# Optimization experiments

Measured on AMD Instinct MI355X. Metric: run time of the kernel, lower is better.

Reference implementation:

```python
import jax, jax.numpy as jnp
import numpy as np

DIM = 512
HEADS = 8
HEAD_DIM = DIM // HEADS
HIDDEN = 4 * DIM
EPS = 1e-5


def _ln(x, g, b):
    mu = jnp.mean(x, axis=-1, keepdims=True)
    var = jnp.mean((x - mu) ** 2, axis=-1, keepdims=True)
    return (x - mu) * jax.lax.rsqrt(var + EPS) * g + b


def setup_inputs() -> dict:
    key = jax.random.key(0)
    ks = jax.random.split(key, 12)
    s = lambda fan: 1.0 / np.sqrt(fan)
    return {
        "x": jax.random.normal(ks[0], (2, 4096, DIM), jnp.float32),
        "ln1_g": jnp.ones((DIM,), jnp.float32),
        "ln1_b": jnp.zeros((DIM,), jnp.float32),
        "ln2_g": jnp.ones((DIM,), jnp.float32),
        "ln2_b": jnp.zeros((DIM,), jnp.float32),
        "qkv_w": jax.random.normal(ks[1], (3 * DIM, DIM), jnp.float32) * s(DIM),
        "qkv_b": jnp.zeros((3 * DIM,), jnp.float32),
        "proj_w": jax.random.normal(ks[2], (DIM, DIM), jnp.float32) * s(DIM),
        "proj_b": jnp.zeros((DIM,), jnp.float32),
        "fc1_w": jax.random.normal(ks[3], (HIDDEN, DIM), jnp.float32) * s(DIM),
        "fc1_b": jnp.zeros((HIDDEN,), jnp.float32),
        "fc2_w": jax.random.normal(ks[4], (DIM, HIDDEN), jnp.float32) * s(HIDDEN),
        "fc2_b": jnp.zeros((DIM,), jnp.float32),
    }


def reference(x, ln1_g, ln1_b, ln2_g, ln2_b, qkv_w, qkv_b, proj_w, proj_b,
              fc1_w, fc1_b, fc2_w, fc2_b):
    B, N, C = x.shape
    # --- attention (pre-norm) ---
    h = _ln(x, ln1_g, ln1_b)
    qkv = h @ qkv_w.T + qkv_b                      # [B,N,3C]
    qkv = qkv.reshape(B, N, 3, HEADS, HEAD_DIM)
    q, k, v = (jnp.moveaxis(qkv, 2, 0)[i].transpose(0, 2, 1, 3) for i in range(3))  # [B,H,N,D]
    scale = HEAD_DIM ** -0.5
    attn = jax.nn.softmax(jnp.einsum('bhnd,bhmd->bhnm', q, k) * scale, axis=-1)
    out = jnp.einsum('bhnm,bhmd->bhnd', attn, v)   # [B,H,N,D]
    out = out.transpose(0, 2, 1, 3).reshape(B, N, C)
    x = x + out @ proj_w.T + proj_b
    # --- MLP (pre-norm) ---
    h = _ln(x, ln2_g, ln2_b)
    h = jax.nn.gelu(h @ fc1_w.T + fc1_b, approximate=False)
    return x + h @ fc2_w.T + fc2_b
```

## Files before the change

kernel.cpp:

```cpp
#include <hip/hip_runtime.h>
#include <hip/hip_bf16.h>
#include <string.h>

using bf16 = __hip_bfloat16;
typedef __attribute__((ext_vector_type(8))) short short8;
typedef __attribute__((ext_vector_type(4))) float f32x4;

#define GAS __attribute__((address_space(1)))
#define LAS __attribute__((address_space(3)))

__device__ __forceinline__ void gld_lds16(const void* g, void* l) {
  __builtin_amdgcn_global_load_lds((const GAS void*)g, (LAS void*)l, 16, 0, 0);
}

__device__ __forceinline__ unsigned short f2bfu(float f) {
  bf16 h = __float2bfloat16(f);
  return *reinterpret_cast<unsigned short*>(&h);
}

__device__ __forceinline__ unsigned pack_bf16x2(float lo, float hi) {
  __hip_bfloat162 v = __float22bfloat162_rn(make_float2(lo, hi));
  unsigned u;
  __builtin_memcpy(&u, &v, 4);
  return u;
}

__global__ __launch_bounds__(256) void cvt_all(const float* __restrict__ w0, bf16* __restrict__ o0,
                                               const float* __restrict__ w1, bf16* __restrict__ o1,
                                               const float* __restrict__ w2, bf16* __restrict__ o2,
                                               const float* __restrict__ w3, bf16* __restrict__ o3) {
  int i = blockIdx.x * 256 + threadIdx.x;
  const float* src; bf16* dst; int off;
  if (i < 196608)      { src = w0; dst = o0; off = i; }
  else if (i < 262144) { src = w1; dst = o1; off = i - 196608; }
  else if (i < 524288) { src = w2; dst = o2; off = i - 262144; }
  else                 { src = w3; dst = o3; off = i - 524288; }
  float4 v = reinterpret_cast<const float4*>(src)[off];
  ushort4 o;
  o.x = f2bfu(v.x); o.y = f2bfu(v.y); o.z = f2bfu(v.z); o.w = f2bfu(v.w);
  reinterpret_cast<ushort4*>(dst)[off] = o;
}

__global__ __launch_bounds__(256) void ln_kernel(const float* __restrict__ x,
                                                 const float* __restrict__ g,
                                                 const float* __restrict__ b,
                                                 bf16* __restrict__ out) {
  const int row = blockIdx.x * 4 + (threadIdx.x >> 6);
  const int lane = threadIdx.x & 63;
  const float4* xr = reinterpret_cast<const float4*>(x + (size_t)row * 512);
  float4 v0 = xr[lane], v1 = xr[64 + lane];
  float s  = v0.x + v0.y + v0.z + v0.w + v1.x + v1.y + v1.z + v1.w;
  float s2 = v0.x*v0.x + v0.y*v0.y + v0.z*v0.z + v0.w*v0.w
           + v1.x*v1.x + v1.y*v1.y + v1.z*v1.z + v1.w*v1.w;
  #pragma unroll
  for (int d = 1; d < 64; d <<= 1) { s += __shfl_xor(s, d); s2 += __shfl_xor(s2, d); }
  const float mu = s * (1.0f / 512.0f);
  const float var = s2 * (1.0f / 512.0f) - mu * mu;
  const float rstd = rsqrtf(var + 1e-5f);
  const float4* g4 = reinterpret_cast<const float4*>(g);
  const float4* b4 = reinterpret_cast<const float4*>(b);
  float4 ga = g4[lane], gb = g4[64 + lane], ba = b4[lane], bb = b4[64 + lane];
  ushort4 o0, o1;
  o0.x = f2bfu((v0.x - mu) * rstd * ga.x + ba.x);
  o0.y = f2bfu((v0.y - mu) * rstd * ga.y + ba.y);
  o0.z = f2bfu((v0.z - mu) * rstd * ga.z + ba.z);
  o0.w = f2bfu((v0.w - mu) * rstd * ga.w + ba.w);
  o1.x = f2bfu((v1.x - mu) * rstd * gb.x + bb.x);
  o1.y = f2bfu((v1.y - mu) * rstd * gb.y + bb.y);
  o1.z = f2bfu((v1.z - mu) * rstd * gb.z + bb.z);
  o1.w = f2bfu((v1.w - mu) * rstd * gb.w + bb.w);
  ushort4* orow = reinterpret_cast<ushort4*>(out + (size_t)row * 512);
  orow[lane] = o0;
  orow[64 + lane] = o1;
}

template <int EPI>
__global__ __launch_bounds__(256) void gemm_bt(const bf16* __restrict__ A,
                                               const bf16* __restrict__ B,
                                               const float* __restrict__ bias,
                                               const float* __restrict__ resid,
                                               void* __restrict__ Cv,
                                               int M, int N, int K) {
  __shared__ bf16 As[128 * 32];
  __shared__ bf16 Bs[128 * 32];
  const int tid = threadIdx.x;
  const int lane = tid & 63, wid = tid >> 6;
  const int lr = lane & 15, lg = lane >> 4;
  const int row0 = blockIdx.x * 128, col0 = blockIdx.y * 128;
  const int wr = (wid >> 1) * 64, wc = (wid & 1) * 64;
  f32x4 acc[4][4] = {};
  const int r1 = tid >> 2,          c1 = (tid & 3) * 8;
  const int r2 = (256 + tid) >> 2,  c2 = ((256 + tid) & 3) * 8;
  for (int kt = 0; kt < K; kt += 32) {
    __syncthreads();
    gld_lds16(A + (size_t)(row0 + r1) * K + kt + c1, As + tid * 8);
    gld_lds16(A + (size_t)(row0 + r2) * K + kt + c2, As + (256 + tid) * 8);
    gld_lds16(B + (size_t)(col0 + r1) * K + kt + c1, Bs + tid * 8);
    gld_lds16(B + (size_t)(col0 + r2) * K + kt + c2, Bs + (256 + tid) * 8);
    __syncthreads();
    short8 af[4], bfr[4];
    #pragma unroll
    for (int mi = 0; mi < 4; ++mi)
      af[mi] = *reinterpret_cast<const short8*>(&As[(wr + mi * 16 + lr) * 32 + lg * 8]);
    #pragma unroll
    for (int nj = 0; nj < 4; ++nj)
      bfr[nj] = *reinterpret_cast<const short8*>(&Bs[(wc + nj * 16 + lr) * 32 + lg * 8]);
    #pragma unroll
    for (int mi = 0; mi < 4; ++mi)
      #pragma unroll
      for (int nj = 0; nj < 4; ++nj)
        acc[mi][nj] = __builtin_amdgcn_mfma_f32_16x16x32_bf16(af[mi], bfr[nj], acc[mi][nj], 0, 0, 0);
  }
  #pragma unroll
  for (int mi = 0; mi < 4; ++mi) {
    #pragma unroll
    for (int nj = 0; nj < 4; ++nj) {
      const int col = col0 + wc + nj * 16 + lr;
      const float bv = bias ? bias[col] : 0.0f;
      #pragma unroll
      for (int rg = 0; rg < 4; ++rg) {
        const int row = row0 + wr + mi * 16 + lg * 4 + rg;
        float v = acc[mi][nj][rg] + bv;
        if constexpr (EPI == 1) v = 0.5f * v * (1.0f + erff(v * 0.70710678118654752f));
        if constexpr (EPI == 2) {
          reinterpret_cast<float*>(Cv)[(size_t)row * N + col] = v + resid[(size_t)row * N + col];
        } else {
          reinterpret_cast<bf16*>(Cv)[(size_t)row * N + col] = __float2bfloat16(v);
        }
      }
    }
  }
}

template <int EPI>
__global__ __launch_bounds__(256) void gemm_bt64(const bf16* __restrict__ A,
                                                 const bf16* __restrict__ B,
                                                 const float* __restrict__ bias,
                                                 const float* __restrict__ resid,
                                                 void* __restrict__ Cv,
                                                 int M, int N, int K) {
  __shared__ bf16 As[64 * 64];
  __shared__ bf16 Bs[64 * 64];
  const int tid = threadIdx.x;
  const int lane = tid & 63, wid = tid >> 6;
  const int lr = lane & 15, lg = lane >> 4;
  const int row0 = blockIdx.x * 64, col0 = blockIdx.y * 64;
  const int wr = (wid >> 1) * 32, wc = (wid & 1) * 32;
  f32x4 acc[2][2] = {};
  const int xsw = (lr & 7) << 4;
  const int fb0 = lr * 128 + ((lg * 16) ^ xsw);
  const int fb1 = lr * 128 + ((64 + lg * 16) ^ xsw);
  const int ph0 = tid * 16, ph1 = (256 + tid) * 16;
  const int r0 = ph0 >> 7, r1 = ph1 >> 7;
  const int lb0 = ph0 ^ ((r0 & 7) << 4), lb1 = ph1 ^ ((r1 & 7) << 4);
  const char* Ab0 = (const char*)A + (size_t)(row0 + r0) * K * 2 + (lb0 & 127);
  const char* Ab1 = (const char*)A + (size_t)(row0 + r1) * K * 2 + (lb1 & 127);
  const char* Bb0 = (const char*)B + (size_t)(col0 + r0) * K * 2 + (lb0 & 127);
  const char* Bb1 = (const char*)B + (size_t)(col0 + r1) * K * 2 + (lb1 & 127);
  for (int kt = 0; kt < K; kt += 64) {
    __syncthreads();
    gld_lds16(Ab0 + kt * 2, (char*)As + ph0);
    gld_lds16(Ab1 + kt * 2, (char*)As + ph1);
    gld_lds16(Bb0 + kt * 2, (char*)Bs + ph0);
    gld_lds16(Bb1 + kt * 2, (char*)Bs + ph1);
    __syncthreads();
    short8 af0[2], af1[2], bf0[2], bf1[2];
    #pragma unroll
    for (int mi = 0; mi < 2; ++mi) {
      af0[mi] = *reinterpret_cast<const short8*>((const char*)As + (wr + mi * 16) * 128 + fb0);
      af1[mi] = *reinterpret_cast<const short8*>((const char*)As + (wr + mi * 16) * 128 + fb1);
    }
    #pragma unroll
    for (int nj = 0; nj < 2; ++nj) {
      bf0[nj] = *reinterpret_cast<const short8*>((const char*)Bs + (wc + nj * 16) * 128 + fb0);
      bf1[nj] = *reinterpret_cast<const short8*>((const char*)Bs + (wc + nj * 16) * 128 + fb1);
    }
    #pragma unroll
    for (int mi = 0; mi < 2; ++mi)
      #pragma unroll
      for (int nj = 0; nj < 2; ++nj) {
        acc[mi][nj] = __builtin_amdgcn_mfma_f32_16x16x32_bf16(af0[mi], bf0[nj], acc[mi][nj], 0, 0, 0);
        acc[mi][nj] = __builtin_amdgcn_mfma_f32_16x16x32_bf16(af1[mi], bf1[nj], acc[mi][nj], 0, 0, 0);
      }
  }
  #pragma unroll
  for (int mi = 0; mi < 2; ++mi) {
    #pragma unroll
    for (int nj = 0; nj < 2; ++nj) {
      const int col = col0 + wc + nj * 16 + lr;
      const float bv = bias ? bias[col] : 0.0f;
      #pragma unroll
      for (int rg = 0; rg < 4; ++rg) {
        const int row = row0 + wr + mi * 16 + lg * 4 + rg;
        float v = acc[mi][nj][rg] + bv;
        if constexpr (EPI == 1) v = 0.5f * v * (1.0f + erff(v * 0.70710678118654752f));
        if constexpr (EPI == 2) {
          reinterpret_cast<float*>(Cv)[(size_t)row * N + col] = v + resid[(size_t)row * N + col];
        } else {
          reinterpret_cast<bf16*>(Cv)[(size_t)row * N + col] = __float2bfloat16(v);
        }
      }
    }
  }
}

__global__ __launch_bounds__(256) void reshape_qkv(const bf16* __restrict__ C,
                                                   bf16* __restrict__ q,
                                                   bf16* __restrict__ k,
                                                   bf16* __restrict__ vf) {
  const int nt = blockIdx.x;
  const int bh = blockIdx.y;
  const int b = bh >> 3, h = bh & 7;
  __shared__ bf16 vs[64][65];
  const int tid = threadIdx.x;
  const float qs = 0.125f * 1.44269504088896340736f;
  #pragma unroll
  for (int i = 0; i < 16; ++i) {
    const int idx = i * 256 + tid;
    const int rr = idx >> 6, c = idx & 63;
    const size_t crow = ((size_t)b * 4096 + nt * 64 + rr) * 1536;
    const size_t onb = ((size_t)bh * 4096 + nt * 64 + rr) * 64 + c;
    q[onb] = __float2bfloat16(__bfloat162float(C[crow + h * 64 + c]) * qs);
    k[onb] = C[crow + 512 + h * 64 + c];
    vs[c][rr] = C[crow + 1024 + h * 64 + c];
  }
  __syncthreads();
  #pragma unroll
  for (int i = 0; i < 2; ++i) {
    const int slot = i * 256 + tid;
    const int db = slot >> 7, kk = (slot >> 6) & 1, l = slot & 63;
    const int lr = l & 15, lg = l >> 4;
    const short8 wv = *reinterpret_cast<const short8*>(&vs[db * 16 + lr][kk * 32 + lg * 8]);
    bf16* dst = vf + ((size_t)bh * 64 + nt) * 4096 + (size_t)(db * 2 + kk) * 512 + l * 8;
    *reinterpret_cast<short8*>(dst) = wv;
  }
}

__global__ __launch_bounds__(256, 4) void attn_kernel(const bf16* __restrict__ Q,
                                                      const bf16* __restrict__ K,
                                                      const bf16* __restrict__ Vf,
                                                      bf16* __restrict__ Out) {
  const int qt = blockIdx.x;
  const int bh = blockIdx.y;
  const int b = bh >> 3, h = bh & 7;
  __shared__ bf16 QP[4096];
  __shared__ bf16 Ks[2][4096];
  const int tid = threadIdx.x, wid = tid >> 6, lane = tid & 63;
  const int lr = lane & 15, lg = lane >> 4;
  const int xsw = (lr & 7) << 4;
  const int fb0 = lr * 128 + ((lg * 16) ^ xsw);
  const int fb1 = lr * 128 + ((64 + lg * 16) ^ xsw);
  const char* Qg = (const char*)(Q + ((size_t)bh * 4096 + qt * 64) * 64);
  const char* Kg = (const char*)(K + (size_t)bh * 4096 * 64);
  const char* vlb = (const char*)Vf + (size_t)bh * 524288 + lane * 16;
  const int ph0 = tid * 16, ph1 = (256 + tid) * 16;
  const int sr0 = ph0 >> 7, sr1 = ph1 >> 7;
  const int lb0 = ph0 ^ ((sr0 & 7) << 4), lb1 = ph1 ^ ((sr1 & 7) << 4);
  int vK0 = lb0, vK1 = lb1;

  gld_lds16(Qg + lb0, (char*)QP + ph0);
  gld_lds16(Qg + lb1, (char*)QP + ph1);
  gld_lds16(Kg + vK0, (char*)Ks[0] + ph0);
  gld_lds16(Kg + vK1, (char*)Ks[0] + ph1);
  vK0 += 8192; vK1 += 8192;
  __syncthreads();
  const char* bpA0 = (const char*)QP + wid * 2048 + fb0;
  const char* bpA1 = (const char*)QP + wid * 2048 + fb1;
  const short8 bq0 = *reinterpret_cast<const short8*>(bpA0);
  const short8 bq1 = *reinterpret_cast<const short8*>(bpA1);
  char* pwp[4];
  #pragma unroll
  for (int nk = 0; nk < 4; ++nk)
    pwp[nk] = (char*)QP + wid * 2048 + lr * 128 + ((nk * 32 + lg * 8) ^ xsw);

  f32x4 Oa[4] = {};
  float mrow = -1e30f, lrow = 0.0f;
  int toff = 0;

#define ATTN_STAGE(BUF) do {                                   \
    gld_lds16(Kg + vK0, (char*)Ks[BUF] + ph0);                 \
    gld_lds16(Kg + vK1, (char*)Ks[BUF] + ph1);                 \
    vK0 += 8192; vK1 += 8192;                                  \
  } while (0)

#define ATTN_COMPUTE(BUF) do {                                                       \
    short8 av0[4], av1[4];                                                           \
    _Pragma("unroll")                                                                \
    for (int db = 0; db < 4; ++db) {                                                 \
      av0[db] = *reinterpret_cast<const short8*>(vlb + toff + db * 2048);            \
      av1[db] = *reinterpret_cast<const short8*>(vlb + toff + db * 2048 + 1024);     \
    }                                                                                \
    toff += 8192;                                                                    \
    const char* ksb = (const char*)Ks[BUF];                                          \
    short8 ak0[4], ak1[4];                                                           \
    _Pragma("unroll")                                                                \
    for (int nk = 0; nk < 4; ++nk) {                                                 \
      ak0[nk] = *reinterpret_cast<const short8*>(ksb + nk * 2048 + fb0);             \
      ak1[nk] = *reinterpret_cast<const short8*>(ksb + nk * 2048 + fb1);             \
    }                                                                                \
    f32x4 Sa[4];                                                                     \
    __builtin_amdgcn_s_setprio(1);                                                   \
    _Pragma("unroll")                                                                \
    for (int nk = 0; nk < 4; ++nk) {                                                 \
      f32x4 z = {0.0f, 0.0f, 0.0f, 0.0f};                                            \
      z = __builtin_amdgcn_mfma_f32_16x16x32_bf16(ak0[nk], bq0, z, 0, 0, 0);         \
      Sa[nk] = __builtin_amdgcn_mfma_f32_16x16x32_bf16(ak1[nk], bq1, z, 0, 0, 0);    \
    }                                                                                \
    __builtin_amdgcn_s_setprio(0);                                                   \
    float t0 = fmaxf(fmaxf(Sa[0][0], Sa[0][1]), fmaxf(Sa[0][2], Sa[0][3]));          \
    float t1 = fmaxf(fmaxf(Sa[1][0], Sa[1][1]), fmaxf(Sa[1][2], Sa[1][3]));          \
    float t2 = fmaxf(fmaxf(Sa[2][0], Sa[2][1]), fmaxf(Sa[2][2], Sa[2][3]));          \
    float t3 = fmaxf(fmaxf(Sa[3][0], Sa[3][1]), fmaxf(Sa[3][2], Sa[3][3]));          \
    float rmax = fmaxf(fmaxf(t0, t1), fmaxf(t2, t3));                                \
    rmax = fmaxf(rmax, __shfl_xor(rmax, 16));                                        \
    rmax = fmaxf(rmax, __shfl_xor(rmax, 32));                                        \
    if (!__all(rmax <= mrow + 8.0f)) {                                               \
      const float mnew = fmaxf(mrow, rmax);                                          \
      const float fsc = __builtin_amdgcn_exp2f(mrow - mnew);                         \
      lrow *= fsc;                                                                   \
      _Pragma("unroll")                                                              \
      for (int db = 0; db < 4; ++db) {                                               \
        Oa[db][0] *= fsc; Oa[db][1] *= fsc; Oa[db][2] *= fsc; Oa[db][3] *= fsc;      \
      }                                                                              \
      mrow = mnew;                                                                   \
    }                                                                                \
    _Pragma("unroll")                                                                \
    for (int nk = 0; nk < 4; ++nk) {                                                 \
      Sa[nk][0] = __builtin_amdgcn_exp2f(Sa[nk][0] - mrow);                          \
      Sa[nk][1] = __builtin_amdgcn_exp2f(Sa[nk][1] - mrow);                          \
      Sa[nk][2] = __builtin_amdgcn_exp2f(Sa[nk][2] - mrow);                          \
      Sa[nk][3] = __builtin_amdgcn_exp2f(Sa[nk][3] - mrow);                          \
    }                                                                                \
    float s0 = (Sa[0][0] + Sa[0][1]) + (Sa[0][2] + Sa[0][3]);                        \
    float s1 = (Sa[1][0] + Sa[1][1]) + (Sa[1][2] + Sa[1][3]);                        \
    float s2 = (Sa[2][0] + Sa[2][1]) + (Sa[2][2] + Sa[2][3]);                        \
    float s3 = (Sa[3][0] + Sa[3][1]) + (Sa[3][2] + Sa[3][3]);                        \
    float rsum = (s0 + s1) + (s2 + s3);                                              \
    rsum += __shfl_xor(rsum, 16);                                                    \
    rsum += __shfl_xor(rsum, 32);                                                    \
    lrow += rsum;                                                                    \
    _Pragma("unroll")                                                                \
    for (int nk = 0; nk < 4; ++nk) {                                                 \
      *reinterpret_cast<unsigned*>(pwp[nk])     = pack_bf16x2(Sa[nk][0], Sa[nk][1]); \
      *reinterpret_cast<unsigned*>(pwp[nk] + 4) = pack_bf16x2(Sa[nk][2], Sa[nk][3]); \
    }                                                                                \
    const short8 bp0 = *reinterpret_cast<const short8*>(bpA0);                       \
    const short8 bp1 = *reinterpret_cast<const short8*>(bpA1);                       \
    __builtin_amdgcn_s_setprio(1);                                                   \
    _Pragma("unroll")                                                                \
    for (int db = 0; db < 4; ++db) {                                                 \
      Oa[db] = __builtin_amdgcn_mfma_f32_16x16x32_bf16(av0[db], bp0, Oa[db], 0, 0, 0); \
      Oa[db] = __builtin_amdgcn_mfma_f32_16x16x32_bf16(av1[db], bp1, Oa[db], 0, 0, 0); \
    }                                                                                \
    __builtin_amdgcn_s_setprio(0);                                                   \
  } while (0)

  for (int tt = 0; tt < 31; ++tt) {
    __syncthreads();
    ATTN_STAGE(1);
    ATTN_COMPUTE(0);
    __syncthreads();
    ATTN_STAGE(0);
    ATTN_COMPUTE(1);
  }
  __syncthreads();
  ATTN_STAGE(1);
  ATTN_COMPUTE(0);
  __syncthreads();
  ATTN_COMPUTE(1);

#undef ATTN_STAGE
#undef ATTN_COMPUTE

  const float linv = 1.0f / lrow;
  const int n = qt * 64 + wid * 16 + lr;
  #pragma unroll
  for (int db = 0; db < 4; ++db) {
    uint2 st;
    st.x = pack_bf16x2(Oa[db][0] * linv, Oa[db][1] * linv);
    st.y = pack_bf16x2(Oa[db][2] * linv, Oa[db][3] * linv);
    *reinterpret_cast<uint2*>(Out + ((size_t)b * 4096 + n) * 512 + h * 64 + db * 16 + lg * 4) = st;
  }
}

extern "C" void kernel_launch(void* const* d_in, const int* in_sizes, int n_in,
                              void* d_out, int out_size, void* d_ws, size_t ws_size,
                              hipStream_t stream) {
  const float* x      = (const float*)d_in[0];
  const float* ln1_g  = (const float*)d_in[1];
  const float* ln1_b  = (const float*)d_in[2];
  const float* ln2_g  = (const float*)d_in[3];
  const float* ln2_b  = (const float*)d_in[4];
  const float* qkv_w  = (const float*)d_in[5];
  const float* qkv_b  = (const float*)d_in[6];
  const float* proj_w = (const float*)d_in[7];
  const float* proj_b = (const float*)d_in[8];
  const float* fc1_w  = (const float*)d_in[9];
  const float* fc1_b  = (const float*)d_in[10];
  const float* fc2_w  = (const float*)d_in[11];
  const float* fc2_b  = (const float*)d_in[12];

  char* ws = (char*)d_ws;
  constexpr size_t o_qkvw = 0;
  constexpr size_t o_projw = 1572864;
  constexpr size_t o_fc1w  = 2097152;
  constexpr size_t o_fc2w  = 4194304;
  constexpr size_t o_h     = 6291456;
  constexpr size_t o_qkvC  = 14680064;
  constexpr size_t o_q     = 39845888;
  constexpr size_t o_k     = 48234496;
  constexpr size_t o_vt    = 56623104;
  constexpr size_t o_attn  = 65011712;
  constexpr size_t o_x2    = 73400320;
  constexpr size_t o_fc1o  = o_qkvC;
  constexpr size_t needed  = 90177536;
  if (ws_size < needed) return;

  bf16* qkvw_bf = (bf16*)(ws + o_qkvw);
  bf16* projw_bf = (bf16*)(ws + o_projw);
  bf16* fc1w_bf = (bf16*)(ws + o_fc1w);
  bf16* fc2w_bf = (bf16*)(ws + o_fc2w);
  bf16* h    = (bf16*)(ws + o_h);
  bf16* qkvC = (bf16*)(ws + o_qkvC);
  bf16* q    = (bf16*)(ws + o_q);
  bf16* k    = (bf16*)(ws + o_k);
  bf16* vf   = (bf16*)(ws + o_vt);
  bf16* attn = (bf16*)(ws + o_attn);
  float* x2  = (float*)(ws + o_x2);
  bf16* fc1o = (bf16*)(ws + o_fc1o);
  float* out = (float*)d_out;

  cvt_all<<<3072, 256, 0, stream>>>(qkv_w, qkvw_bf, proj_w, projw_bf, fc1_w, fc1w_bf, fc2_w, fc2w_bf);

  ln_kernel<<<2048, 256, 0, stream>>>(x, ln1_g, ln1_b, h);
  gemm_bt<0><<<dim3(64, 12), 256, 0, stream>>>(h, qkvw_bf, qkv_b, nullptr, qkvC, 8192, 1536, 512);
  reshape_qkv<<<dim3(64, 16), 256, 0, stream>>>(qkvC, q, k, vf);
  attn_kernel<<<dim3(64, 16), 256, 0, stream>>>(q, k, vf, attn);
  gemm_bt64<2><<<dim3(128, 8), 256, 0, stream>>>(attn, projw_bf, proj_b, x, x2, 8192, 512, 512);
  ln_kernel<<<2048, 256, 0, stream>>>(x2, ln2_g, ln2_b, h);
  gemm_bt<1><<<dim3(64, 16), 256, 0, stream>>>(h, fc1w_bf, fc1_b, nullptr, fc1o, 8192, 2048, 512);
  gemm_bt64<2><<<dim3(128, 8), 256, 0, stream>>>(fc1o, fc2w_bf, fc2_b, x2, out, 8192, 512, 2048);
}
```

Before: 265.9 us.

## Rewrite attention with 32x32 MFMA, split-KV wave pairs, register-resident P

The attention kernel moves from 16x16x32 to 32x32x16 bf16 MFMA tiles. Each pair of waves splits the KV sequence in half for a 32-row query group, and the two partial softmax states are merged through LDS at the end. The P matrix stays in registers as the MFMA B operand, split into hi and lo bf16 parts, which removes the LDS round trip for P but doubles the PV MFMA count. The V reshape layout is changed to match the new fragment order, and K staging now loads two KV halves per stage.

```diff
diff --git a/kernel.cpp b/kernel.cpp
--- a/kernel.cpp
+++ b/kernel.cpp
@@ -5,6 +5,7 @@
 using bf16 = __hip_bfloat16;
 typedef __attribute__((ext_vector_type(8))) short short8;
 typedef __attribute__((ext_vector_type(4))) float f32x4;
+typedef __attribute__((ext_vector_type(16))) float f32x16;
 
 #define GAS __attribute__((address_space(1)))
 #define LAS __attribute__((address_space(3)))
@@ -211,7 +212,7 @@
   const int nt = blockIdx.x;
   const int bh = blockIdx.y;
   const int b = bh >> 3, h = bh & 7;
-  __shared__ bf16 vs[64][65];
+  __shared__ alignas(16) bf16 vs[64][72];
   const int tid = threadIdx.x;
   const float qs = 0.125f * 1.44269504088896340736f;
   #pragma unroll
@@ -227,12 +228,17 @@
   __syncthreads();
   #pragma unroll
   for (int i = 0; i < 2; ++i) {
-    const int slot = i * 256 + tid;
-    const int db = slot >> 7, kk = (slot >> 6) & 1, l = slot & 63;
-    const int lr = l & 15, lg = l >> 4;
-    const short8 wv = *reinterpret_cast<const short8*>(&vs[db * 16 + lr][kk * 32 + lg * 8]);
-    bf16* dst = vf + ((size_t)bh * 64 + nt) * 4096 + (size_t)(db * 2 + kk) * 512 + l * 8;
-    *reinterpret_cast<short8*>(dst) = wv;
+    const int s = i * 256 + tid;
+    const int half = (s >> 8) & 1, db = (s >> 7) & 1, c = (s >> 6) & 1, l = s & 63;
+    const int d = db * 32 + (l & 31);
+    const int n0 = half * 32 + c * 16 + ((l >> 5) << 2);
+    const short4 lo = *reinterpret_cast<const short4*>(&vs[d][n0]);
+    const short4 hi = *reinterpret_cast<const short4*>(&vs[d][n0 + 8]);
+    short8 v;
+    v[0] = lo.x; v[1] = lo.y; v[2] = lo.z; v[3] = lo.w;
+    v[4] = hi.x; v[5] = hi.y; v[6] = hi.z; v[7] = hi.w;
+    bf16* dst = vf + ((size_t)bh * 128 + nt * 2 + half) * 2048 + (db * 2 + c) * 512 + (size_t)l * 8;
+    *reinterpret_cast<short8*>(dst) = v;
   }
 }
 
@@ -243,143 +249,169 @@
   const int qt = blockIdx.x;
   const int bh = blockIdx.y;
   const int b = bh >> 3, h = bh & 7;
-  __shared__ bf16 QP[4096];
-  __shared__ bf16 Ks[2][4096];
-  const int tid = threadIdx.x, wid = tid >> 6, lane = tid & 63;
-  const int lr = lane & 15, lg = lane >> 4;
-  const int xsw = (lr & 7) << 4;
-  const int fb0 = lr * 128 + ((lg * 16) ^ xsw);
-  const int fb1 = lr * 128 + ((64 + lg * 16) ^ xsw);
-  const char* Qg = (const char*)(Q + ((size_t)bh * 4096 + qt * 64) * 64);
-  const char* Kg = (const char*)(K + (size_t)bh * 4096 * 64);
-  const char* vlb = (const char*)Vf + (size_t)bh * 524288 + lane * 16;
-  const int ph0 = tid * 16, ph1 = (256 + tid) * 16;
-  const int sr0 = ph0 >> 7, sr1 = ph1 >> 7;
-  const int lb0 = ph0 ^ ((sr0 & 7) << 4), lb1 = ph1 ^ ((sr1 & 7) << 4);
-  int vK0 = lb0, vK1 = lb1;
-
-  gld_lds16(Qg + lb0, (char*)QP + ph0);
-  gld_lds16(Qg + lb1, (char*)QP + ph1);
-  gld_lds16(Kg + vK0, (char*)Ks[0] + ph0);
-  gld_lds16(Kg + vK1, (char*)Ks[0] + ph1);
-  vK0 += 8192; vK1 += 8192;
+  __shared__ alignas(16) char smem[17408];
+  const int tid = threadIdx.x, w = tid >> 6, lane = tid & 63;
+  const int qg = w >> 1, kvh = w & 1;
+  const int l31 = lane & 31, hi = lane >> 5;
+
+  const bf16* qrow = Q + ((size_t)bh * 4096 + qt * 64 + qg * 32 + l31) * 64 + hi * 8;
+  const short8 qf0 = *reinterpret_cast<const short8*>(qrow);
+  const short8 qf1 = *reinterpret_cast<const short8*>(qrow + 16);
+  const short8 qf2 = *reinterpret_cast<const short8*>(qrow + 32);
+  const short8 qf3 = *reinterpret_cast<const short8*>(qrow + 48);
+
+  const char* KgB = (const char*)K + (size_t)bh * 524288;
+  const int php = tid * 16;
+  const int rowp = php >> 7;
+  const int lbp = php ^ ((rowp & 7) << 4);
+  const int xswl = (lane & 7) << 4;
+  const int fk0 = l31 * 128 + (( 0 + hi * 16) ^ xswl);
+  const int fk1 = l31 * 128 + ((32 + hi * 16) ^ xswl);
+  const int fk2 = l31 * 128 + ((64 + hi * 16) ^ xswl);
+  const int fk3 = l31 * 128 + ((96 + hi * 16) ^ xswl);
+  const int kvh4096 = kvh * 4096;
+  const char* vwp = (const char*)Vf + ((size_t)bh * 128 + (size_t)kvh * 64) * 4096 + lane * 16;
+
+  f32x16 O0 = {}, O1 = {};
+  float mrow = -1e30f, lrow = 0.0f;
+
+  gld_lds16(KgB + lbp, smem + php);
+  gld_lds16(KgB + 262144 + lbp, smem + 4096 + php);
+  int koff = 4096;
+
+  auto stage = [&](int buf) {
+    gld_lds16(KgB + koff + lbp, smem + buf * 8192 + php);
+    gld_lds16(KgB + 262144 + koff + lbp, smem + buf * 8192 + 4096 + php);
+    koff += 4096;
+  };
+
+  auto compute = [&](int buf) {
+    const short8 va00 = *reinterpret_cast<const short8*>(vwp);
+    const short8 va01 = *reinterpret_cast<const short8*>(vwp + 1024);
+    const short8 va10 = *reinterpret_cast<const short8*>(vwp + 2048);
+    const short8 va11 = *reinterpret_cast<const short8*>(vwp + 3072);
+    vwp += 4096;
+    const char* kt = smem + buf * 8192 + kvh4096;
+    const short8 kf0 = *reinterpret_cast<const short8*>(kt + fk0);
+    const short8 kf1 = *reinterpret_cast<const short8*>(kt + fk1);
+    const short8 kf2 = *reinterpret_cast<const short8*>(kt + fk2);
+    const short8 kf3 = *reinterpret_cast<const short8*>(kt + fk3);
+    f32x16 S = {};
+    __builtin_amdgcn_s_setprio(1);
+    S = __builtin_amdgcn_mfma_f32_32x32x16_bf16(kf0, qf0, S, 0, 0, 0);
+    S = __builtin_amdgcn_mfma_f32_32x32x16_bf16(kf1, qf1, S, 0, 0, 0);
+    S = __builtin_amdgcn_mfma_f32_32x32x16_bf16(kf2, qf2, S, 0, 0, 0);
+    S = __builtin_amdgcn_mfma_f32_32x32x16_bf16(kf3, qf3, S, 0, 0, 0);
+    __builtin_amdgcn_s_setprio(0);
+    float a0 = fmaxf(fmaxf(S[0], S[1]), fmaxf(S[2], S[3]));
+    float a1 = fmaxf(fmaxf(S[4], S[5]), fmaxf(S[6], S[7]));
+    float a2 = fmaxf(fmaxf(S[8], S[9]), fmaxf(S[10], S[11]));
+    float a3 = fmaxf(fmaxf(S[12], S[13]), fmaxf(S[14], S[15]));
+    float rmax = fmaxf(fmaxf(a0, a1), fmaxf(a2, a3));
+    float ra = rmax, rb = rmax;
+    asm volatile("v_permlane32_swap_b32 %0, %1" : "+v"(ra), "+v"(rb));
+    rmax = fmaxf(ra, rb);
+    if (!__all(rmax <= mrow + 8.0f)) {
+      const float mnew = fmaxf(mrow, rmax);
+      const float fsc = __builtin_amdgcn_exp2f(mrow - mnew);
+      lrow *= fsc;
+      #pragma unroll
+      for (int i = 0; i < 16; ++i) { O0[i] *= fsc; O1[i] *= fsc; }
+      mrow = mnew;
+    }
+    #pragma unroll
+    for (int i = 0; i < 16; ++i) S[i] = __builtin_amdgcn_exp2f(S[i] - mrow);
+    float s0 = (S[0] + S[1]) + (S[2] + S[3]);
+    float s1 = (S[4] + S[5]) + (S[6] + S[7]);
+    float s2 = (S[8] + S[9]) + (S[10] + S[11]);
+    float s3 = (S[12] + S[13]) + (S[14] + S[15]);
+    float rsum = (s0 + s1) + (s2 + s3);
+    float sa = rsum, sb = rsum;
+    asm volatile("v_permlane32_swap_b32 %0, %1" : "+v"(sa), "+v"(sb));
+    lrow += sa + sb;
+    union U8 { unsigned u[4]; short8 s8; };
+    __builtin_amdgcn_s_setprio(1);
+    {
+      U8 ph, pl;
+      ph.u[0] = pack_bf16x2(S[0], S[1]);  ph.u[1] = pack_bf16x2(S[2], S[3]);
+      ph.u[2] = pack_bf16x2(S[4], S[5]);  ph.u[3] = pack_bf16x2(S[6], S[7]);
+      float lo[8];
+      #pragma unroll
+      for (int e = 0; e < 8; ++e) {
+        unsigned hv = (e & 1) ? (ph.u[e >> 1] & 0xFFFF0000u) : (ph.u[e >> 1] << 16);
+        float hf; __builtin_memcpy(&hf, &hv, 4);
+        lo[e] = S[e] - hf;
+      }
+      pl.u[0] = pack_bf16x2(lo[0], lo[1]); pl.u[1] = pack_bf16x2(lo[2], lo[3]);
+      pl.u[2] = pack_bf16x2(lo[4], lo[5]); pl.u[3] = pack_bf16x2(lo[6], lo[7]);
+      O0 = __builtin_amdgcn_mfma_f32_32x32x16_bf16(va00, ph.s8, O0, 0, 0, 0);
+      O0 = __builtin_amdgcn_mfma_f32_32x32x16_bf16(va00, pl.s8, O0, 0, 0, 0);
+      O1 = __builtin_amdgcn_mfma_f32_32x32x16_bf16(va10, ph.s8, O1, 0, 0, 0);
+      O1 = __builtin_amdgcn_mfma_f32_32x32x16_bf16(va10, pl.s8, O1, 0, 0, 0);
+    }
+    {
+      U8 ph, pl;
+      ph.u[0] = pack_bf16x2(S[8], S[9]);   ph.u[1] = pack_bf16x2(S[10], S[11]);
+      ph.u[2] = pack_bf16x2(S[12], S[13]); ph.u[3] = pack_bf16x2(S[14], S[15]);
+      float lo[8];
+      #pragma unroll
+      for (int e = 0; e < 8; ++e) {
+        unsigned hv = (e & 1) ? (ph.u[e >> 1] & 0xFFFF0000u) : (ph.u[e >> 1] << 16);
+        float hf; __builtin_memcpy(&hf, &hv, 4);
+        lo[e] = S[8 + e] - hf;
+      }
+      pl.u[0] = pack_bf16x2(lo[0], lo[1]); pl.u[1] = pack_bf16x2(lo[2], lo[3]);
+      pl.u[2] = pack_bf16x2(lo[4], lo[5]); pl.u[3] = pack_bf16x2(lo[6], lo[7]);
+      O0 = __builtin_amdgcn_mfma_f32_32x32x16_bf16(va01, ph.s8, O0, 0, 0, 0);
+      O0 = __builtin_amdgcn_mfma_f32_32x32x16_bf16(va01, pl.s8, O0, 0, 0, 0);
+      O1 = __builtin_amdgcn_mfma_f32_32x32x16_bf16(va11, ph.s8, O1, 0, 0, 0);
+      O1 = __builtin_amdgcn_mfma_f32_32x32x16_bf16(va11, pl.s8, O1, 0, 0, 0);
+    }
+    __builtin_amdgcn_s_setprio(0);
+  };
+
+  for (int tt = 0; tt < 31; ++tt) {
+    __syncthreads(); stage(1); compute(0);
+    __syncthreads(); stage(0); compute(1);
+  }
+  __syncthreads(); stage(1); compute(0);
+  __syncthreads(); compute(1);
+
   __syncthreads();
-  const char* bpA0 = (const char*)QP + wid * 2048 + fb0;
-  const char* bpA1 = (const char*)QP + wid * 2048 + fb1;
-  const short8 bq0 = *reinterpret_cast<const short8*>(bpA0);
-  const short8 bq1 = *reinterpret_cast<const short8*>(bpA1);
-  char* pwp[4];
-  #pragma unroll
-  for (int nk = 0; nk < 4; ++nk)
-    pwp[nk] = (char*)QP + wid * 2048 + lr * 128 + ((nk * 32 + lg * 8) ^ xsw);
-
-  f32x4 Oa[4] = {};
-  float mrow = -1e30f, lrow = 0.0f;
-  int toff = 0;
-
-#define ATTN_STAGE(BUF) do {                                   \
-    gld_lds16(Kg + vK0, (char*)Ks[BUF] + ph0);                 \
-    gld_lds16(Kg + vK1, (char*)Ks[BUF] + ph1);                 \
-    vK0 += 8192; vK1 += 8192;                                  \
-  } while (0)
-
-#define ATTN_COMPUTE(BUF) do {                                                       \
-    short8 av0[4], av1[4];                                                           \
-    _Pragma("unroll")                                                                \
-    for (int db = 0; db < 4; ++db) {                                                 \
-      av0[db] = *reinterpret_cast<const short8*>(vlb + toff + db * 2048);            \
-      av1[db] = *reinterpret_cast<const short8*>(vlb + toff + db * 2048 + 1024);     \
-    }                                                                                \
-    toff += 8192;                                                                    \
-    const char* ksb = (const char*)Ks[BUF];                                          \
-    short8 ak0[4], ak1[4];                                                           \
-    _Pragma("unroll")                                                                \
-    for (int nk = 0; nk < 4; ++nk) {                                                 \
-      ak0[nk] = *reinterpret_cast<const short8*>(ksb + nk * 2048 + fb0);             \
-      ak1[nk] = *reinterpret_cast<const short8*>(ksb + nk * 2048 + fb1);             \
-    }                                                                                \
-    f32x4 Sa[4];                                                                     \
-    __builtin_amdgcn_s_setprio(1);                                                   \
-    _Pragma("unroll")                                                                \
-    for (int nk = 0; nk < 4; ++nk) {                                                 \
-      f32x4 z = {0.0f, 0.0f, 0.0f, 0.0f};                                            \
-      z = __builtin_amdgcn_mfma_f32_16x16x32_bf16(ak0[nk], bq0, z, 0, 0, 0);         \
-      Sa[nk] = __builtin_amdgcn_mfma_f32_16x16x32_bf16(ak1[nk], bq1, z, 0, 0, 0);    \
-    }                                                                                \
-    __builtin_amdgcn_s_setprio(0);                                                   \
-    float t0 = fmaxf(fmaxf(Sa[0][0], Sa[0][1]), fmaxf(Sa[0][2], Sa[0][3]));          \
-    float t1 = fmaxf(fmaxf(Sa[1][0], Sa[1][1]), fmaxf(Sa[1][2], Sa[1][3]));          \
-    float t2 = fmaxf(fmaxf(Sa[2][0], Sa[2][1]), fmaxf(Sa[2][2], Sa[2][3]));          \
-    float t3 = fmaxf(fmaxf(Sa[3][0], Sa[3][1]), fmaxf(Sa[3][2], Sa[3][3]));          \
-    float rmax = fmaxf(fmaxf(t0, t1), fmaxf(t2, t3));                                \
-    rmax = fmaxf(rmax, __shfl_xor(rmax, 16));                                        \
-    rmax = fmaxf(rmax, __shfl_xor(rmax, 32));                                        \
-    if (!__all(rmax <= mrow + 8.0f)) {                                               \
-      const float mnew = fmaxf(mrow, rmax);                                          \
-      const float fsc = __builtin_amdgcn_exp2f(mrow - mnew);                         \
-      lrow *= fsc;                                                                   \
-      _Pragma("unroll")                                                              \
-      for (int db = 0; db < 4; ++db) {                                               \
-        Oa[db][0] *= fsc; Oa[db][1] *= fsc; Oa[db][2] *= fsc; Oa[db][3] *= fsc;      \
-      }                                                                              \
-      mrow = mnew;                                                                   \
-    }                                                                                \
-    _Pragma("unroll")                                                                \
-    for (int nk = 0; nk < 4; ++nk) {                                                 \
-      Sa[nk][0] = __builtin_amdgcn_exp2f(Sa[nk][0] - mrow);                          \
-      Sa[nk][1] = __builtin_amdgcn_exp2f(Sa[nk][1] - mrow);                          \
-      Sa[nk][2] = __builtin_amdgcn_exp2f(Sa[nk][2] - mrow);                          \
-      Sa[nk][3] = __builtin_amdgcn_exp2f(Sa[nk][3] - mrow);                          \
-    }                                                                                \
-    float s0 = (Sa[0][0] + Sa[0][1]) + (Sa[0][2] + Sa[0][3]);                        \
-    float s1 = (Sa[1][0] + Sa[1][1]) + (Sa[1][2] + Sa[1][3]);                        \
-    float s2 = (Sa[2][0] + Sa[2][1]) + (Sa[2][2] + Sa[2][3]);                        \
-    float s3 = (Sa[3][0] + Sa[3][1]) + (Sa[3][2] + Sa[3][3]);                        \
-    float rsum = (s0 + s1) + (s2 + s3);                                              \
-    rsum += __shfl_xor(rsum, 16);                                                    \
-    rsum += __shfl_xor(rsum, 32);                                                    \
-    lrow += rsum;                                                                    \
-    _Pragma("unroll")                                                                \
-    for (int nk = 0; nk < 4; ++nk) {                                                 \
-      *reinterpret_cast<unsigned*>(pwp[nk])     = pack_bf16x2(Sa[nk][0], Sa[nk][1]); \
-      *reinterpret_cast<unsigned*>(pwp[nk] + 4) = pack_bf16x2(Sa[nk][2], Sa[nk][3]); \
-    }                                                                                \
-    const short8 bp0 = *reinterpret_cast<const short8*>(bpA0);                       \
-    const short8 bp1 = *reinterpret_cast<const short8*>(bpA1);                       \
-    __builtin_amdgcn_s_setprio(1);                                                   \
-    _Pragma("unroll")                                                                \
-    for (int db = 0; db < 4; ++db) {                                                 \
-      Oa[db] = __builtin_amdgcn_mfma_f32_16x16x32_bf16(av0[db], bp0, Oa[db], 0, 0, 0); \
-      Oa[db] = __builtin_amdgcn_mfma_f32_16x16x32_bf16(av1[db], bp1, Oa[db], 0, 0, 0); \
-    }                                                                                \
-    __builtin_amdgcn_s_setprio(0);                                                   \
-  } while (0)
-
-  for (int tt = 0; tt < 31; ++tt) {
-    __syncthreads();
-    ATTN_STAGE(1);
-    ATTN_COMPUTE(0);
-    __syncthreads();
-    ATTN_STAGE(0);
-    ATTN_COMPUTE(1);
+  float* area = reinterpret_cast<float*>(smem) + qg * 2176;
+  if (kvh) {
+    #pragma unroll
+    for (int r = 0; r < 16; ++r) {
+      area[r * 64 + lane] = O0[r];
+      area[(16 + r) * 64 + lane] = O1[r];
+    }
+    area[2048 + lane] = mrow;
+    area[2112 + lane] = lrow;
   }
   __syncthreads();
-  ATTN_STAGE(1);
-  ATTN_COMPUTE(0);
-  __syncthreads();
-  ATTN_COMPUTE(1);
-
-#undef ATTN_STAGE
-#undef ATTN_COMPUTE
-
-  const float linv = 1.0f / lrow;
-  const int n = qt * 64 + wid * 16 + lr;
-  #pragma unroll
-  for (int db = 0; db < 4; ++db) {
-    uint2 st;
-    st.x = pack_bf16x2(Oa[db][0] * linv, Oa[db][1] * linv);
-    st.y = pack_bf16x2(Oa[db][2] * linv, Oa[db][3] * linv);
-    *reinterpret_cast<uint2*>(Out + ((size_t)b * 4096 + n) * 512 + h * 64 + db * 16 + lg * 4) = st;
+  if (!kvh) {
+    const float mB = area[2048 + lane], lB = area[2112 + lane];
+    const float mx = fmaxf(mrow, mB);
+    const float fa = __builtin_amdgcn_exp2f(mrow - mx);
+    const float fb = __builtin_amdgcn_exp2f(mB - mx);
+    const float inv = 1.0f / (lrow * fa + lB * fb);
+    const int qrow = qt * 64 + qg * 32 + l31;
+    bf16* ob = Out + ((size_t)b * 4096 + qrow) * 512 + h * 64 + hi * 4;
+    #pragma unroll
+    for (int db = 0; db < 2; ++db) {
+      #pragma unroll
+      for (int rq = 0; rq < 4; ++rq) {
+        const int r = rq * 4;
+        float v0 = ((db ? O1[r + 0] : O0[r + 0]) * fa + area[(db * 16 + r + 0) * 64 + lane] * fb) * inv;
+        float v1 = ((db ? O1[r + 1] : O0[r + 1]) * fa + area[(db * 16 + r + 1) * 64 + lane] * fb) * inv;
+        float v2 = ((db ? O1[r + 2] : O0[r + 2]) * fa + area[(db * 16 + r + 2) * 64 + lane] * fb) * inv;
+        float v3 = ((db ? O1[r + 3] : O0[r + 3]) * fa + area[(db * 16 + r + 3) * 64 + lane] * fb) * inv;
+        uint2 st;
+        st.x = pack_bf16x2(v0, v1);
+        st.y = pack_bf16x2(v2, v3);
+        *reinterpret_cast<uint2*>(ob + db * 32 + rq * 8) = st;
+      }
+    }
   }
 }
 
```

Result: slower. 279.3 us (+5.0%).
